# Kernel tuning notes

Measured on AMD Instinct MI355X. Metric: run time of the kernel, lower is better.

The kernel has to match this reference:

```python
import jax, jax.numpy as jnp
import numpy as np

B, S, T, F = 64, 128, 64, 100
EPS = 1e-7  # K.epsilon()


def setup_inputs() -> dict:
    key = jax.random.key(0)
    ks = jax.random.split(key, 6)
    sc = 1.0 / np.sqrt(F)
    return {
        "x": jax.random.normal(ks[0], (B, S, T, F), jnp.float32),
        "W": jax.random.normal(ks[1], (F, F), jnp.float32) * sc,
        "W_context": jax.random.normal(ks[2], (F, F), jnp.float32) * sc,
        "b": jnp.zeros((F,), jnp.float32),
        "u": jax.random.normal(ks[3], (F,), jnp.float32) * sc,
        "Wx": jax.random.normal(ks[4], (F, 3 * F), jnp.float32) * sc,
        "Wh": jax.random.normal(ks[5], (F, 3 * F), jnp.float32) * sc,
        "bg": jnp.zeros((3 * F,), jnp.float32),
    }


def reference(x, W, W_context, b, u, Wx, Wh, bg):
    # x: (B, S, T, F) -> scan over sentence axis S
    Bn, Sn, Tn, Fn = x.shape

    def gru_step(h, a):
        # standard GRU cell: h (B,F), a (B,F)
        gx = a @ Wx + bg          # (B, 3F)
        gh = h @ Wh               # (B, 3F)
        zr = jax.nn.sigmoid(gx[:, : 2 * Fn] + gh[:, : 2 * Fn])
        z, r = zr[:, :Fn], zr[:, Fn:]
        h_tilde = jnp.tanh(gx[:, 2 * Fn :] + r * gh[:, 2 * Fn :])
        return (1.0 - z) * h + z * h_tilde

    def step(h, x_):
        # x_: (B, T, F); h: (B, F) recurrent context
        uit = jnp.tanh(x_ @ W + b + (h @ W_context)[:, None, :])  # (B,T,F)
        ait = uit @ u                                              # (B,T)
        a = jnp.exp(ait)
        a = a / (jnp.sum(a, axis=1, keepdims=True) + EPS)
        attended = jnp.einsum("btf,bt->bf", x_, a)                 # (B,F)
        h_new = gru_step(h, attended)
        return h_new, h_new

    h0 = jnp.zeros((Bn, Fn), x.dtype)
    _, outs = jax.lax.scan(step, h0, jnp.transpose(x, (1, 0, 2, 3)))  # (S,B,F)
    return jnp.transpose(outs, (1, 0, 2))  # (B,S,F)
```

## Files before the change

kernel.cpp:

```cpp
#include <hip/hip_runtime.h>

#define BN 64
#define SN 128
#define TN 64
#define FN 100
#define G3 300

__device__ __forceinline__ float rl(float v, int l){
  return __int_as_float(__builtin_amdgcn_readlane(__float_as_int(v), l));
}
__device__ __forceinline__ float fast_exp(float x){
  return __builtin_amdgcn_exp2f(x * 1.44269504088896341f);
}
__device__ __forceinline__ float fast_tanh(float x){
  float e = __builtin_amdgcn_exp2f(x * 2.88539008177792681f);
  return 1.0f - 2.0f * __builtin_amdgcn_rcpf(1.0f + e);
}
__device__ __forceinline__ float fast_sig(float x){
  return __builtin_amdgcn_rcpf(1.0f + __builtin_amdgcn_exp2f(-1.44269504088896341f * x));
}

#define BARS() asm volatile("s_waitcnt lgkmcnt(0)\n\ts_barrier" ::: "memory")
#define WAIT_VM0() asm volatile("s_waitcnt vmcnt(0)" ::: "memory")

__global__ __launch_bounds__(256) void k_xw(
    const float* __restrict__ x, const float* __restrict__ W,
    const float* __restrict__ b, float* __restrict__ xw)
{
  const int tid  = threadIdx.x;
  const int lane = tid & 63;
  const int c    = __builtin_amdgcn_readfirstlane(tid >> 6);
  const int c25  = c * 25;

  __shared__ float xs[64 * 101];
  const long rowbase = (long)blockIdx.x * 64;
  const float* xsrc = x + rowbase * FN;
  #pragma unroll
  for (int i = 0; i < 25; i++){
    const int o = i * 256 + tid;
    const int r = o / FN;
    const int k = o - r * FN;
    xs[r * 101 + k] = xsrc[o];
  }
  __syncthreads();

  float acc[25];
  const float* bp = b + c25;
  #pragma unroll
  for (int j = 0; j < 25; j++) acc[j] = bp[j];

  const float* Wp = W + c25;
  #pragma unroll 4
  for (int k = 0; k < FN; k++){
    const float xv = xs[lane * 101 + k];
    const float* Wk = Wp + (long)k * FN;
    #pragma unroll
    for (int j = 0; j < 25; j++) acc[j] = fmaf(xv, Wk[j], acc[j]);
  }

  float* op = xw + (rowbase + lane) * FN + c25;
  #pragma unroll
  for (int j = 0; j < 25; j++) op[j] = acc[j];
}

__global__
__attribute__((amdgpu_flat_work_group_size(512, 512)))
__attribute__((amdgpu_waves_per_eu(2, 2)))
void k_scan(
    const float* __restrict__ x, const float* __restrict__ xw,
    const float* __restrict__ Wc, const float* __restrict__ u,
    const float* __restrict__ Wx, const float* __restrict__ Wh,
    const float* __restrict__ bg, float* __restrict__ out)
{
  const int b    = blockIdx.x;
  const int tid  = threadIdx.x;
  const int lane = tid & 63;
  const int wid  = tid >> 6;

  const int gth = tid & 127;
  const int fsl = tid >> 7;
  const int tB  = tid >> 3;
  const int fsB = tid & 7;
  const bool fCv = (tid & 127) < FN;
  const int fC  = fCv ? (tid & 127) : (FN - 1);
  const int tsC = tid >> 7;

  __shared__ __align__(16) float xwbuf[2][TN*FN + 16];
  __shared__ __align__(16) float xbuf[2][TN*FN];
  __shared__ float part5[700][5];
  __shared__ float h_lds[128];
  __shared__ float c_lds[128];
  __shared__ float att_unused[4];
  __shared__ float ea_lds[64];
  __shared__ __align__(16) float dpart[8];

  float wr[25][5];
  float wcr[25];
  const bool hasC = (gth >= 28);
  const int  co   = hasC ? gth - 28 : 0;
  #pragma unroll
  for (int j = 0; j < 25; j++){
    const int f = fsl*25 + j;
    #pragma unroll
    for (int p = 0; p < 5; p++){
      const int o = gth + 128*p;
      wr[j][p] = (o < 600) ? ((o < 300) ? Wx[f*G3 + o] : Wh[f*G3 + (o-300)]) : 0.0f;
    }
    wcr[j] = hasC ? Wc[f*FN + co] : 0.0f;
  }
  float2 ur[7];
  #pragma unroll
  for (int i = 0; i < 7; i++){
    const int f = fsB*14 + 2*i;
    ur[i].x = (f   < FN) ? u[f]   : 0.0f;
    ur[i].y = (f+1 < FN) ? u[f+1] : 0.0f;
  }
  const int gg = (tid < FN) ? tid : 0;
  const float bgz = bg[gg], bgr = bg[FN+gg], bgh = bg[2*FN+gg];

  if (tid < 128){ h_lds[tid] = 0.0f; c_lds[tid] = 0.0f; }
  if (tid < 16){ xwbuf[0][TN*FN + tid] = 0.0f; xwbuf[1][TN*FN + tid] = 0.0f; }
  __syncthreads();

  const long tileStride = (long)TN*FN;
  const float* xw_base = xw + (long)b*SN*tileStride;
  const float* x_base  = x  + (long)b*SN*tileStride;

  auto issue_tile = [&](const float* gsrc, float* ldst){
    const char* g = (const char*)gsrc;
    char* l = (char*)ldst;
    #pragma unroll
    for (int r = 0; r < 4; r++){
      const int chunk = (r*8 + wid) * 1024;
      if (chunk < 25600){
        __builtin_amdgcn_global_load_lds(
          (const __attribute__((address_space(1))) unsigned int*)(g + chunk + lane*16),
          (__attribute__((address_space(3))) unsigned int*)(l + chunk),
          16, 0, 0);
      }
    }
  };

  issue_tile(xw_base, &xwbuf[0][0]);
  issue_tile(x_base,  &xbuf[0][0]);

  for (int s = 0; s < SN; s++){
    float hp = h_lds[fsl*25 + (lane < 25 ? lane : 0)];
    float accC = 0.0f;
    #pragma unroll
    for (int j = 0; j < 25; j++) accC = fmaf(rl(hp, j), wcr[j], accC);
    if (hasC) part5[600 + co][fsl] = accC;
    BARS();

    if (tid < FN)
      c_lds[tid] = part5[600+tid][0] + part5[600+tid][1]
                 + part5[600+tid][2] + part5[600+tid][3];
    WAIT_VM0();
    BARS();

    {
      const float2* cp  = reinterpret_cast<const float2*>(&c_lds[fsB*14]);
      const float2* xp2 = reinterpret_cast<const float2*>(&xwbuf[s&1][tB*FN + fsB*14]);
      float accB = 0.0f;
      #pragma unroll
      for (int i = 0; i < 7; i++){
        float2 cc = cp[i];
        float2 xx = xp2[i];
        accB = fmaf(fast_tanh(xx.x + cc.x), ur[i].x, accB);
        accB = fmaf(fast_tanh(xx.y + cc.y), ur[i].y, accB);
      }
      accB += __shfl_xor(accB, 1);
      accB += __shfl_xor(accB, 2);
      accB += __shfl_xor(accB, 4);
      float ea = fast_exp(accB);
      if (fsB == 0) ea_lds[tB] = ea;
      float dsum = ea;
      dsum += __shfl_xor(dsum, 8);
      dsum += __shfl_xor(dsum, 16);
      dsum += __shfl_xor(dsum, 32);
      if (lane == 0) dpart[wid] = dsum;
    }
    BARS();

    {
      const int sp = (s+1 < SN) ? s+1 : s;
      issue_tile(xw_base + (long)sp*tileStride, &xwbuf[(s+1)&1][0]);
      issue_tile(x_base  + (long)sp*tileStride, &xbuf[(s+1)&1][0]);
    }

    {
      const float* xt = &xbuf[s&1][(long)tsC*(16*FN) + fC];
      const float4* eap = reinterpret_cast<const float4*>(&ea_lds[tsC*16]);
      float4 e0 = eap[0], e1 = eap[1], e2 = eap[2], e3 = eap[3];
      float a = 0.0f;
      a = fmaf(xt[0*FN],  e0.x, a); a = fmaf(xt[1*FN],  e0.y, a);
      a = fmaf(xt[2*FN],  e0.z, a); a = fmaf(xt[3*FN],  e0.w, a);
      a = fmaf(xt[4*FN],  e1.x, a); a = fmaf(xt[5*FN],  e1.y, a);
      a = fmaf(xt[6*FN],  e1.z, a); a = fmaf(xt[7*FN],  e1.w, a);
      a = fmaf(xt[8*FN],  e2.x, a); a = fmaf(xt[9*FN],  e2.y, a);
      a = fmaf(xt[10*FN], e2.z, a); a = fmaf(xt[11*FN], e2.w, a);
      a = fmaf(xt[12*FN], e3.x, a); a = fmaf(xt[13*FN], e3.y, a);
      a = fmaf(xt[14*FN], e3.z, a); a = fmaf(xt[15*FN], e3.w, a);
      if (fCv) part5[600 + fC][tsC] = a;
    }
    BARS();

    {
      const float4* dp4 = reinterpret_cast<const float4*>(dpart);
      float4 d0 = dp4[0], d1 = dp4[1];
      float den = d0.x+d0.y+d0.z+d0.w + d1.x+d1.y+d1.z+d1.w + 1e-7f;
      float rden = 1.0f / den;
      const int fA = fsl*25 + (lane < 25 ? lane : 0);
      float attp = (part5[600+fA][0] + part5[600+fA][1]
                  + part5[600+fA][2] + part5[600+fA][3]) * rden;
      const bool p2x = (gth < 44);
      float a0=0.f, a1=0.f, a2=0.f, a3=0.f, a4=0.f;
      #pragma unroll
      for (int j = 0; j < 25; j++){
        float sa = rl(attp, j);
        float sh = rl(hp, j);
        float s2 = p2x ? sa : sh;
        a0 = fmaf(sa, wr[j][0], a0);
        a1 = fmaf(sa, wr[j][1], a1);
        a2 = fmaf(s2, wr[j][2], a2);
        a3 = fmaf(sh, wr[j][3], a3);
        a4 = fmaf(sh, wr[j][4], a4);
      }
      part5[gth      ][fsl] = a0;
      part5[gth + 128][fsl] = a1;
      part5[gth + 256][fsl] = a2;
      part5[gth + 384][fsl] = a3;
      if (gth < 88) part5[gth + 512][fsl] = a4;
    }
    BARS();

    if (tid < FN){
      const int g = tid;
      float gxz = part5[g    ][0]+part5[g    ][1]+part5[g    ][2]+part5[g    ][3] + bgz;
      float gxr = part5[100+g][0]+part5[100+g][1]+part5[100+g][2]+part5[100+g][3] + bgr;
      float gxh = part5[200+g][0]+part5[200+g][1]+part5[200+g][2]+part5[200+g][3] + bgh;
      float ghz = part5[300+g][0]+part5[300+g][1]+part5[300+g][2]+part5[300+g][3];
      float ghr = part5[400+g][0]+part5[400+g][1]+part5[400+g][2]+part5[400+g][3];
      float ghh = part5[500+g][0]+part5[500+g][1]+part5[500+g][2]+part5[500+g][3];
      float z  = fast_sig(gxz + ghz);
      float r  = fast_sig(gxr + ghr);
      float ht = fast_tanh(gxh + r*ghh);
      float hn = (1.0f - z)*h_lds[g] + z*ht;
      h_lds[g] = hn;
      out[((long)b*SN + s)*FN + g] = hn;
    }
    BARS();
  }
}

extern "C" void kernel_launch(void* const* d_in, const int* in_sizes, int n_in,
                              void* d_out, int out_size, void* d_ws, size_t ws_size,
                              hipStream_t stream)
{
  const float* x  = (const float*)d_in[0];
  const float* W  = (const float*)d_in[1];
  const float* Wc = (const float*)d_in[2];
  const float* bb = (const float*)d_in[3];
  const float* u  = (const float*)d_in[4];
  const float* Wx = (const float*)d_in[5];
  const float* Wh = (const float*)d_in[6];
  const float* bg = (const float*)d_in[7];
  float* out = (float*)d_out;
  float* xwbuf = (float*)d_ws;

  k_xw  <<<dim3((BN*SN*TN)/64), dim3(256), 0, stream>>>(x, W, bb, xwbuf);
  k_scan<<<dim3(BN), dim3(512), 0, stream>>>(x, xwbuf, Wc, u, Wx, Wh, bg, out);
}
```

Measured before the change: 954.2 us.

## Keep W in registers for x@W and broadcast x rows via readlane

The x@W precompute kernel is rewritten so each wave holds the full weight matrix in registers, 200 floats per lane, instead of reading W from global memory for every row. Rows of x are streamed into registers with one group prefetched ahead, and each row element is broadcast across the wave with readlane. The grid becomes 512 blocks, each wave covering 256 rows. The scan kernel also pins its register-resident weights with empty asm so the compiler does not rematerialize or reload them. The costs are very high register pressure, one wave per EU, and a large number of serial readlane operations.

```diff
diff --git a/kernel.cpp b/kernel.cpp
--- a/kernel.cpp
+++ b/kernel.cpp
@@ -22,45 +22,64 @@
 
 #define BARS() asm volatile("s_waitcnt lgkmcnt(0)\n\ts_barrier" ::: "memory")
 #define WAIT_VM0() asm volatile("s_waitcnt vmcnt(0)" ::: "memory")
-
-__global__ __launch_bounds__(256) void k_xw(
+#define PIN(v) asm volatile("" : "+v"(v))
+
+__global__
+__attribute__((amdgpu_flat_work_group_size(256, 256)))
+__attribute__((amdgpu_waves_per_eu(1)))
+void k_xw(
     const float* __restrict__ x, const float* __restrict__ W,
     const float* __restrict__ b, float* __restrict__ xw)
 {
   const int tid  = threadIdx.x;
   const int lane = tid & 63;
-  const int c    = __builtin_amdgcn_readfirstlane(tid >> 6);
-  const int c25  = c * 25;
-
-  __shared__ float xs[64 * 101];
-  const long rowbase = (long)blockIdx.x * 64;
-  const float* xsrc = x + rowbase * FN;
-  #pragma unroll
-  for (int i = 0; i < 25; i++){
-    const int o = i * 256 + tid;
-    const int r = o / FN;
-    const int k = o - r * FN;
-    xs[r * 101 + k] = xsrc[o];
-  }
-  __syncthreads();
-
-  float acc[25];
-  const float* bp = b + c25;
-  #pragma unroll
-  for (int j = 0; j < 25; j++) acc[j] = bp[j];
-
-  const float* Wp = W + c25;
-  #pragma unroll 4
-  for (int k = 0; k < FN; k++){
-    const float xv = xs[lane * 101 + k];
-    const float* Wk = Wp + (long)k * FN;
-    #pragma unroll
-    for (int j = 0; j < 25; j++) acc[j] = fmaf(xv, Wk[j], acc[j]);
-  }
-
-  float* op = xw + (rowbase + lane) * FN + c25;
-  #pragma unroll
-  for (int j = 0; j < 25; j++) op[j] = acc[j];
+  const int wid  = tid >> 6;
+  const long rowBase = ((long)blockIdx.x * 4 + wid) * 256;
+
+  const bool hasB = (lane < 36);
+  const int  cb   = hasB ? 64 + lane : 64;
+  float wA[FN], wB[FN];
+  #pragma unroll
+  for (int f = 0; f < FN; f++){
+    wA[f] = W[f*FN + lane];
+    wB[f] = W[f*FN + cb];
+  }
+  #pragma unroll
+  for (int f = 0; f < FN; f++){ PIN(wA[f]); PIN(wB[f]); }
+  const float ba  = b[lane];
+  const float bb2 = hasB ? b[64 + lane] : 0.0f;
+
+  const float* xp = x + rowBase * FN;
+  float xg[13], xh[13];
+  #pragma unroll
+  for (int r = 0; r < 13; r++)
+    xg[r] = (r*64 + lane < 800) ? xp[r*64 + lane] : 0.0f;
+
+  #pragma unroll 1
+  for (int grp = 0; grp < 32; grp++){
+    if (grp < 31){
+      const float* xq = xp + (grp+1)*800;
+      #pragma unroll
+      for (int r = 0; r < 13; r++)
+        xh[r] = (r*64 + lane < 800) ? xq[r*64 + lane] : 0.0f;
+    }
+    #pragma unroll
+    for (int g = 0; g < 8; g++){
+      float accA = ba, accB = bb2;
+      #pragma unroll
+      for (int f = 0; f < FN; f++){
+        const int idx = g*FN + f;
+        float s = rl(xg[idx >> 6], idx & 63);
+        accA = fmaf(s, wA[f], accA);
+        accB = fmaf(s, wB[f], accB);
+      }
+      const long row = rowBase + grp*8 + g;
+      xw[row*FN + lane] = accA;
+      if (hasB) xw[row*FN + 64 + lane] = accB;
+    }
+    #pragma unroll
+    for (int r = 0; r < 13; r++) xg[r] = xh[r];
+  }
 }
 
 __global__
@@ -90,7 +109,6 @@
   __shared__ float part5[700][5];
   __shared__ float h_lds[128];
   __shared__ float c_lds[128];
-  __shared__ float att_unused[4];
   __shared__ float ea_lds[64];
   __shared__ __align__(16) float dpart[8];
 
@@ -116,7 +134,17 @@
     ur[i].y = (f+1 < FN) ? u[f+1] : 0.0f;
   }
   const int gg = (tid < FN) ? tid : 0;
-  const float bgz = bg[gg], bgr = bg[FN+gg], bgh = bg[2*FN+gg];
+  float bgz = bg[gg], bgr = bg[FN+gg], bgh = bg[2*FN+gg];
+
+  #pragma unroll
+  for (int j = 0; j < 25; j++){
+    #pragma unroll
+    for (int p = 0; p < 5; p++) PIN(wr[j][p]);
+    PIN(wcr[j]);
+  }
+  #pragma unroll
+  for (int i = 0; i < 7; i++){ PIN(ur[i].x); PIN(ur[i].y); }
+  PIN(bgz); PIN(bgr); PIN(bgh);
 
   if (tid < 128){ h_lds[tid] = 0.0f; c_lds[tid] = 0.0f; }
   if (tid < 16){ xwbuf[0][TN*FN + tid] = 0.0f; xwbuf[1][TN*FN + tid] = 0.0f; }
@@ -268,6 +296,6 @@
   float* out = (float*)d_out;
   float* xwbuf = (float*)d_ws;
 
-  k_xw  <<<dim3((BN*SN*TN)/64), dim3(256), 0, stream>>>(x, W, bb, xwbuf);
+  k_xw  <<<dim3((BN*SN*TN)/1024), dim3(256), 0, stream>>>(x, W, bb, xwbuf);
   k_scan<<<dim3(BN), dim3(512), 0, stream>>>(x, xwbuf, Wc, u, Wx, Wh, bg, out);
 }
```

After: 1.055 ms. 1.11x slower.
